# Performance work log

Hardware: AMD Instinct MI355X
Metric: run time of the kernel (lower is better)

The kernel has to match this reference:

```python
import jax, jax.numpy as jnp
import numpy as np

MARGIN = 0.2
LAMBDA_LSE = 6.0
LAMBDA_SOFTMAX = 9.0
EPS = 1e-8


def setup_inputs() -> dict:
    key = jax.random.key(0)
    k1, k2, k3 = jax.random.split(key, 3)
    I, R, W, D = 128, 36, 24, 512
    images = jax.random.normal(k1, (I, R, D), dtype=jnp.float32)
    captions = jax.random.normal(k2, (I, W, D), dtype=jnp.float32)
    # ragged caption lengths in [4, 24]
    cap_lens = 4 + jax.random.randint(k3, (I,), 0, W - 3, dtype=jnp.int32)
    return {"images": images, "captions": captions, "cap_lens": cap_lens}


def _scan_t2i_loss(images, captions, cap_lens):
    # images: [I, R, D]; captions: [C, W, D]; cap_lens: [C]
    C, W, D = captions.shape
    wmask = jnp.arange(W)[None, :] < cap_lens[:, None]          # [C, W] valid-word mask

    # raw attention: bmm(context=images, query^T=caption) -> [C, I, R, W]
    attn = jnp.einsum('ird,cwd->cirw', images, captions)
    # clipped_l2norm: LeakyReLU(0.1) then l2-normalize over word axis;
    # zero padded words so norms match the per-caption sliced computation
    a = jnp.where(attn > 0, attn, 0.1 * attn) * wmask[:, None, None, :]
    a = a / (jnp.sqrt(jnp.sum(a * a, axis=3, keepdims=True)) + EPS)
    # softmax over regions (sourceL) with temperature lambda_softmax
    s = jax.nn.softmax(a * LAMBDA_SOFTMAX, axis=2)              # [C, I, R, W]
    # weighted context per word: [C, I, W, D]
    wei = jnp.einsum('cirw,ird->ciwd', s, images)

    cap = captions[:, None, :, :]                               # [C, 1, W, D]
    num = jnp.sum(cap * wei, axis=-1)                           # [C, I, W]
    den = jnp.clip(jnp.linalg.norm(cap, axis=-1) * jnp.linalg.norm(wei, axis=-1), EPS)
    cos = num / den                                             # [C, I, W]

    # LogSumExp aggregation over valid words
    neg = jnp.finfo(cos.dtype).min
    logits = jnp.where(wmask[:, None, :], cos * LAMBDA_LSE, neg)
    row_sim = jax.nn.logsumexp(logits, axis=-1) / LAMBDA_LSE    # [C, I]
    scores = row_sim.T                                          # [I, C] (image x caption)

    diag = jnp.diag(scores)[:, None]                            # [I, 1]
    cost_s = jnp.clip(MARGIN + scores - diag, 0.0)
    cost_im = jnp.clip(MARGIN + scores - diag.T, 0.0)
    eye = jnp.eye(scores.shape[0], dtype=bool)
    cost_s = jnp.where(eye, 0.0, cost_s)
    cost_im = jnp.where(eye, 0.0, cost_im)
    # max_violation=True: hardest negatives
    cost_s = jnp.max(cost_s, axis=1)
    cost_im = jnp.max(cost_im, axis=0)
    return jnp.sum(cost_s) + jnp.sum(cost_im)


def reference(images, captions, cap_lens):
    return _scan_t2i_loss(images, captions, cap_lens)
```

## Files before the change

### kernel.cpp

```cpp
#include <hip/hip_runtime.h>
#include <math.h>

#define I_N 128
#define C_N 128
#define R_N 36
#define W_N 24
#define D_N 512
#define M_N (I_N * R_N)
#define N_N (C_N * W_N)

typedef __attribute__((ext_vector_type(8))) short bf16x8;
typedef __attribute__((ext_vector_type(4))) float f32x4;
typedef __attribute__((ext_vector_type(8))) unsigned short u16x8;
typedef _Float16 f16x2 __attribute__((ext_vector_type(2)));
typedef __fp16 h16x2 __attribute__((ext_vector_type(2)));

__device__ inline float bf2f(unsigned short u) {
    return __uint_as_float(((unsigned int)u) << 16);
}
__device__ inline unsigned short f2bf(float f) {
    unsigned int u = __float_as_uint(f);
    u = (u + 0x7FFFu + ((u >> 16) & 1u)) >> 16;
    return (unsigned short)u;
}
__device__ inline void gload_lds16(const void* g, void* l) {
    __builtin_amdgcn_global_load_lds(
        (const __attribute__((address_space(1))) void*)g,
        (__attribute__((address_space(3))) void*)l, 16, 0, 0);
}

#if __has_builtin(__builtin_amdgcn_fdot2)
__device__ inline float fdot2f(f16x2 a, f16x2 b, float c) {
    return __builtin_amdgcn_fdot2(__builtin_bit_cast(h16x2, a),
                                  __builtin_bit_cast(h16x2, b), c, false);
}
#else
__device__ inline float fdot2f(f16x2 a, f16x2 b, float c) {
    return c + (float)a[0] * (float)b[0] + (float)a[1] * (float)b[1];
}
#endif

#if __has_builtin(__builtin_amdgcn_cvt_pkrtz)
__device__ inline f16x2 pkf16(float a, float b) {
    return __builtin_bit_cast(f16x2, __builtin_amdgcn_cvt_pkrtz(a, b));
}
#else
__device__ inline f16x2 pkf16(float a, float b) {
    f16x2 v; v[0] = (_Float16)a; v[1] = (_Float16)b; return v;
}
#endif

__global__ __launch_bounds__(256) void convert_kernel(const float* __restrict__ images,
                                                      const float* __restrict__ captions,
                                                      unsigned short* __restrict__ imgbf,
                                                      unsigned short* __restrict__ capbf,
                                                      float* __restrict__ capn) {
    const int bid = blockIdx.x;
    if (bid < 1152) {
        int idx = bid * 256 + threadIdx.x;
        float4 v0 = *(const float4*)(images + (size_t)idx * 8);
        float4 v1 = *(const float4*)(images + (size_t)idx * 8 + 4);
        u16x8 o;
        o[0] = f2bf(v0.x); o[1] = f2bf(v0.y); o[2] = f2bf(v0.z); o[3] = f2bf(v0.w);
        o[4] = f2bf(v1.x); o[5] = f2bf(v1.y); o[6] = f2bf(v1.z); o[7] = f2bf(v1.w);
        *(u16x8*)(imgbf + (size_t)idx * 8) = o;
    } else {
        const int crow = (bid - 1152) * 4 + (threadIdx.x >> 6);
        const int lane = threadIdx.x & 63;
        const float* p = captions + (size_t)crow * D_N + lane * 8;
        float4 v0 = *(const float4*)p;
        float4 v1 = *(const float4*)(p + 4);
        u16x8 o;
        o[0] = f2bf(v0.x); o[1] = f2bf(v0.y); o[2] = f2bf(v0.z); o[3] = f2bf(v0.w);
        o[4] = f2bf(v1.x); o[5] = f2bf(v1.y); o[6] = f2bf(v1.z); o[7] = f2bf(v1.w);
        *(u16x8*)(capbf + (size_t)crow * D_N + lane * 8) = o;
        float s = v0.x*v0.x + v0.y*v0.y + v0.z*v0.z + v0.w*v0.w
                + v1.x*v1.x + v1.y*v1.y + v1.z*v1.z + v1.w*v1.w;
        #pragma unroll
        for (int off = 32; off > 0; off >>= 1) s += __shfl_down(s, off);
        if (lane == 0) capn[crow] = sqrtf(s);
    }
}

__global__ __launch_bounds__(256) void gram_kernel(const float* __restrict__ images,
                                                   unsigned int* __restrict__ G2) {
    __shared__ float tile[R_N][68];
    __shared__ float gshf[R_N][R_N];
    const int i = blockIdx.x;
    const float* img = images + (size_t)i * R_N * D_N;
    const int tid = threadIdx.x;
    const int t1 = (tid / 12) * 3;
    const int t2 = (tid % 12) * 3;
    const bool active = tid < 144;
    float acc[3][3] = {{0.f,0.f,0.f},{0.f,0.f,0.f},{0.f,0.f,0.f}};
    for (int k0 = 0; k0 < D_N; k0 += 64) {
        for (int idx = tid; idx < R_N * 16; idx += 256) {
            int r = idx / 16, k4 = idx % 16;
            float4 v = *(const float4*)(img + (size_t)r * D_N + k0 + k4 * 4);
            *(float4*)&tile[r][k4 * 4] = v;
        }
        __syncthreads();
        if (active) {
            #pragma unroll
            for (int k = 0; k < 64; k += 4) {
                float4 a0 = *(const float4*)&tile[t1 + 0][k];
                float4 a1 = *(const float4*)&tile[t1 + 1][k];
                float4 a2 = *(const float4*)&tile[t1 + 2][k];
                float4 b0 = *(const float4*)&tile[t2 + 0][k];
                float4 b1 = *(const float4*)&tile[t2 + 1][k];
                float4 b2 = *(const float4*)&tile[t2 + 2][k];
                acc[0][0] += a0.x*b0.x + a0.y*b0.y + a0.z*b0.z + a0.w*b0.w;
                acc[0][1] += a0.x*b1.x + a0.y*b1.y + a0.z*b1.z + a0.w*b1.w;
                acc[0][2] += a0.x*b2.x + a0.y*b2.y + a0.z*b2.z + a0.w*b2.w;
                acc[1][0] += a1.x*b0.x + a1.y*b0.y + a1.z*b0.z + a1.w*b0.w;
                acc[1][1] += a1.x*b1.x + a1.y*b1.y + a1.z*b1.z + a1.w*b1.w;
                acc[1][2] += a1.x*b2.x + a1.y*b2.y + a1.z*b2.z + a1.w*b2.w;
                acc[2][0] += a2.x*b0.x + a2.y*b0.y + a2.z*b0.z + a2.w*b0.w;
                acc[2][1] += a2.x*b1.x + a2.y*b1.y + a2.z*b1.z + a2.w*b1.w;
                acc[2][2] += a2.x*b2.x + a2.y*b2.y + a2.z*b2.z + a2.w*b2.w;
            }
        }
        __syncthreads();
    }
    if (active) {
        #pragma unroll
        for (int a = 0; a < 3; ++a)
            #pragma unroll
            for (int b = 0; b < 3; ++b)
                gshf[t1 + a][t2 + b] = acc[a][b];
    }
    __syncthreads();
    unsigned int* gp = G2 + (size_t)i * (R_N * 18);
    for (int idx = tid; idx < R_N * 18; idx += 256) {
        int r = idx / 18, p = idx % 18;
        gp[idx] = __builtin_bit_cast(unsigned int, pkf16(gshf[r][2 * p], gshf[r][2 * p + 1]));
    }
}

#define BM 128
#define BN 128
#define BK 32
#define KT (D_N / BK)
#define GX (M_N / BM)
#define GY (N_N / BN)

__global__ __launch_bounds__(256, 4) void attn_gemm_kernel(const unsigned short* __restrict__ A,
                                                           const unsigned short* __restrict__ B,
                                                           unsigned short* __restrict__ attn) {
    __shared__ unsigned short AsBuf[2][BM * BK];
    __shared__ unsigned short BsBuf[2][BN * BK];
    const int flat = blockIdx.x;
    const int nf = (flat & 7) * (GX * GY / 8) + (flat >> 3);
    const int m0 = (nf / GY) * BM;
    const int n0 = (nf % GY) * BN;
    const int tid = threadIdx.x;
    const int lane = tid & 63;
    const int wid = tid >> 6;
    const int wr = wid >> 1, wc = wid & 1;
    const int fr = lane & 15;
    const int fk = lane >> 4;

    const int srow = tid >> 2;
    const int sslot = (tid & 3) ^ (srow & 3);
    const unsigned short* srcA = A + (size_t)(m0 + srow) * D_N + sslot * 8;
    const unsigned short* srcB = B + (size_t)(n0 + srow) * D_N + sslot * 8;
    const int ldst = tid * 16;

    f32x4 acc[4][4];
    #pragma unroll
    for (int m = 0; m < 4; ++m)
        #pragma unroll
        for (int n = 0; n < 4; ++n) acc[m][n] = (f32x4){0.f, 0.f, 0.f, 0.f};

    #define STAGE(t, buf)                                                              \
        {                                                                              \
            const unsigned short* _a = srcA + (t) * BK;                                \
            const unsigned short* _b = srcB + (t) * BK;                                \
            gload_lds16(_a, (char*)AsBuf[buf] + ldst);                                 \
            gload_lds16(_a + (size_t)64 * D_N, (char*)AsBuf[buf] + 4096 + ldst);       \
            gload_lds16(_b, (char*)BsBuf[buf] + ldst);                                 \
            gload_lds16(_b + (size_t)64 * D_N, (char*)BsBuf[buf] + 4096 + ldst);       \
        }

    STAGE(0, 0)
    STAGE(1, 1)
    asm volatile("s_waitcnt vmcnt(4)" ::: "memory");
    __builtin_amdgcn_sched_barrier(0);
    __builtin_amdgcn_s_barrier();
    __builtin_amdgcn_sched_barrier(0);

    #pragma unroll
    for (int t = 0; t < KT; ++t) {
        const int cur = t & 1;
        const unsigned short* As = AsBuf[cur];
        const unsigned short* Bs = BsBuf[cur];
        bf16x8 af[4], bfr[4];
        #pragma unroll
        for (int m = 0; m < 4; ++m) {
            int rl = wr * 64 + m * 16 + fr;
            int byt = rl * 64 + ((fk ^ (fr & 3)) << 4);
            af[m] = *(const bf16x8*)((const char*)As + byt);
        }
        #pragma unroll
        for (int n = 0; n < 4; ++n) {
            int rl = wc * 64 + n * 16 + fr;
            int byt = rl * 64 + ((fk ^ (fr & 3)) << 4);
            bfr[n] = *(const bf16x8*)((const char*)Bs + byt);
        }
        #pragma unroll
        for (int m = 0; m < 4; ++m)
            #pragma unroll
            for (int n = 0; n < 4; ++n)
                acc[m][n] = __builtin_amdgcn_mfma_f32_16x16x32_bf16(af[m], bfr[n], acc[m][n], 0, 0, 0);
        __builtin_amdgcn_sched_barrier(0);
        __builtin_amdgcn_s_barrier();
        __builtin_amdgcn_sched_barrier(0);
        if (t + 2 < KT) STAGE(t + 2, cur)
        if (t + 1 < KT) {
            if (t + 2 < KT) {
                asm volatile("s_waitcnt vmcnt(4)" ::: "memory");
            } else {
                asm volatile("s_waitcnt vmcnt(0)" ::: "memory");
            }
            __builtin_amdgcn_sched_barrier(0);
            __builtin_amdgcn_s_barrier();
            __builtin_amdgcn_sched_barrier(0);
        }
    }
    #undef STAGE

    #pragma unroll
    for (int m = 0; m < 4; ++m) {
        #pragma unroll
        for (int n = 0; n < 4; ++n) {
            #pragma unroll
            for (int j = 0; j < 4; ++j) {
                int row = m0 + wr * 64 + m * 16 + fk * 4 + j;
                int col = n0 + wc * 64 + n * 16 + fr;
                int i = row / R_N, r = row - i * R_N;
                int c = col / W_N, w = col - c * W_N;
                attn[(((size_t)i * C_N + c) * R_N + r) * W_N + w] = f2bf(acc[m][n][j]);
            }
        }
    }
}

#define CG 8
#define SCL9 12.98425537f

__global__ __launch_bounds__(192) void score_kernel(const unsigned short* __restrict__ attn,
                                                    const unsigned int* __restrict__ G2,
                                                    const float* __restrict__ capn,
                                                    const int* __restrict__ cap_lens,
                                                    float* __restrict__ scores) {
    __shared__ unsigned short stage[CG * R_N * W_N];
    __shared__ unsigned int gsh2[R_N * 18];
    __shared__ float scl_sh[CG * R_N];
    __shared__ float red[CG][W_N];
    __shared__ int len_sh[CG];
    const int i = blockIdx.x;
    const int c0 = blockIdx.y * CG;
    const int tid = threadIdx.x;

    if (tid < CG) len_sh[tid] = cap_lens[c0 + tid];
    const unsigned short* at = attn + ((size_t)i * C_N + c0) * R_N * W_N;
    for (int ch = tid; ch < CG * R_N * W_N / 8; ch += 192)
        *(u16x8*)&stage[ch * 8] = *(const u16x8*)(at + ch * 8);
    const unsigned int* gp = G2 + (size_t)i * (R_N * 18);
    for (int idx = tid; idx < R_N * 18 / 2; idx += 192)
        *(uint2*)&gsh2[idx * 2] = *(const uint2*)(gp + idx * 2);
    __syncthreads();

    for (int row = tid; row < CG * R_N; row += 192) {
        int cl = row / R_N;
        int len = len_sh[cl];
        const unsigned short* rp = &stage[row * W_N];
        u16x8 p0 = *(const u16x8*)&rp[0];
        u16x8 p1 = *(const u16x8*)&rp[8];
        u16x8 p2 = *(const u16x8*)&rp[16];
        float ss = 0.f;
        #pragma unroll
        for (int q = 0; q < 8; ++q) {
            float x0 = bf2f(p0[q]); x0 = x0 > 0.f ? x0 : 0.1f * x0; x0 = (q      < len) ? x0 : 0.f;
            float x1 = bf2f(p1[q]); x1 = x1 > 0.f ? x1 : 0.1f * x1; x1 = (q + 8  < len) ? x1 : 0.f;
            float x2 = bf2f(p2[q]); x2 = x2 > 0.f ? x2 : 0.1f * x2; x2 = (q + 16 < len) ? x2 : 0.f;
            ss += x0 * x0 + x1 * x1 + x2 * x2;
        }
        scl_sh[row] = SCL9 / (sqrtf(ss) + 1e-8f);
    }
    __syncthreads();

    {
        const int cl = tid / W_N, w = tid - cl * W_N;
        const int len = len_sh[cl];
        const bool valid = w < len;
        const unsigned short* sb = &stage[cl * R_N * W_N];
        const float* sclp = &scl_sh[cl * R_N];
        f16x2 ep[18];
        float Z = 0.f, nu = 0.f;
        float e_prev = 0.f;
        #pragma unroll
        for (int r = 0; r < R_N; ++r) {
            float raw = bf2f(sb[r * W_N + w]);
            float x = raw > 0.f ? raw : 0.1f * raw;
            float l = valid ? x * sclp[r] : 0.f;
            float e = exp2f(l);
            Z += e;
            nu += e * raw;
            if (r & 1) ep[r >> 1] = pkf16(e_prev, e);
            else e_prev = e;
        }
        float wn = 0.f;
        #pragma unroll
        for (int r2 = 0; r2 < R_N; ++r2) {
            const unsigned int* grow = &gsh2[r2 * 18];
            float t0 = 0.f, t1 = 0.f;
            #pragma unroll
            for (int p = 0; p < 18; ++p) {
                f16x2 g = __builtin_bit_cast(f16x2, grow[p]);
                if (p & 1) t1 = fdot2f(g, ep[p], t1);
                else       t0 = fdot2f(g, ep[p], t0);
            }
            wn += (t0 + t1) * (float)ep[r2 >> 1][r2 & 1];
        }
        float iZ = 1.f / Z;
        float cn = capn[(c0 + cl) * W_N + w];
        float den = fmaxf(cn * sqrtf(fmaxf(wn, 0.f)) * iZ, 1e-8f);
        red[cl][w] = valid ? (nu * iZ) / den * 6.0f : -3.4e38f;
    }
    __syncthreads();
    if (tid < CG) {
        float se = 0.f;
        #pragma unroll
        for (int w = 0; w < W_N; ++w) se += __expf(red[tid][w] - 6.0f);
        scores[(size_t)(c0 + tid) * I_N + i] = (__logf(se) + 6.0f) / 6.0f;
    }
}

__global__ __launch_bounds__(128) void final_kernel(const float* __restrict__ scores,
                                                    float* __restrict__ out) {
    __shared__ float diag[C_N];
    __shared__ float red[C_N];
    const int t = threadIdx.x;
    diag[t] = scores[t * C_N + t];
    __syncthreads();
    const float di = diag[t];
    float cs = 0.f, cim = 0.f;
    for (int k = 0; k < C_N; ++k) {
        if (k == t) continue;
        float vs = 0.2f + scores[k * C_N + t] - di;
        float vi = 0.2f + scores[t * C_N + k] - di;
        cs = fmaxf(cs, vs);
        cim = fmaxf(cim, vi);
    }
    red[t] = cs + cim;
    __syncthreads();
    #pragma unroll
    for (int off = 64; off > 0; off >>= 1) {
        if (t < off) red[t] += red[t + off];
        __syncthreads();
    }
    if (t == 0) out[0] = red[0];
}

extern "C" void kernel_launch(void* const* d_in, const int* in_sizes, int n_in,
                              void* d_out, int out_size, void* d_ws, size_t ws_size,
                              hipStream_t stream) {
    (void)in_sizes; (void)n_in; (void)out_size; (void)ws_size;
    const float* images = (const float*)d_in[0];
    const float* captions = (const float*)d_in[1];
    const int* cap_lens = (const int*)d_in[2];
    float* out = (float*)d_out;

    char* wsb = (char*)d_ws;
    size_t off = 0;
    auto alloc = [&](size_t bytes) -> char* {
        char* p = wsb + off;
        off += (bytes + 255) & ~(size_t)255;
        return p;
    };
    unsigned short* imgbf = (unsigned short*)alloc((size_t)M_N * D_N * 2);
    unsigned short* capbf = (unsigned short*)alloc((size_t)N_N * D_N * 2);
    unsigned int* G2 = (unsigned int*)alloc((size_t)I_N * R_N * 18 * 4);
    float* capn = (float*)alloc((size_t)C_N * W_N * 4);
    float* scores = (float*)alloc((size_t)C_N * I_N * 4);
    unsigned short* attn = (unsigned short*)alloc((size_t)I_N * C_N * R_N * W_N * 2);

    convert_kernel<<<1920, 256, 0, stream>>>(images, captions, imgbf, capbf, capn);
    gram_kernel<<<I_N, 256, 0, stream>>>(images, G2);
    attn_gemm_kernel<<<GX * GY, 256, 0, stream>>>(imgbf, capbf, attn);
    score_kernel<<<dim3(I_N, C_N / CG), 192, 0, stream>>>(attn, G2, capn, cap_lens, scores);
    final_kernel<<<1, 128, 0, stream>>>(scores, out);
}
```

Measured before the change: 118.1 us.

## Fuse attention GEMM with score computation, keeping attention tile in shared memory

Merges the attention GEMM and score kernels into one kernel. Each block computes a 144x192 tile covering 4 images by 8 captions, writes the bf16 result to LDS, and then runs normalization, softmax, the weighted-norm and the LSE reduction in place, so the large attention tensor is never written to or read back from global memory. The Gram rows are padded to 20 words so they can be read with vector loads. The tradeoff is a larger LDS footprint (about 79 KB) and higher register pressure from 27 accumulators and three words per thread, which drops occupancy to 2 blocks. The per-wave vmcnt waits are also made uneven to match the extra A loads issued by wave 0.

After: 350.2 us. +196.4%, slower.

```diff
diff --git a/kernel.cpp b/kernel.cpp
--- a/kernel.cpp
+++ b/kernel.cpp
@@ -130,61 +130,94 @@
                 gshf[t1 + a][t2 + b] = acc[a][b];
     }
     __syncthreads();
-    unsigned int* gp = G2 + (size_t)i * (R_N * 18);
-    for (int idx = tid; idx < R_N * 18; idx += 256) {
-        int r = idx / 18, p = idx % 18;
-        gp[idx] = __builtin_bit_cast(unsigned int, pkf16(gshf[r][2 * p], gshf[r][2 * p + 1]));
-    }
-}
-
-#define BM 128
-#define BN 128
+    unsigned int* gp = G2 + (size_t)i * (R_N * 20);
+    for (int idx = tid; idx < R_N * 20; idx += 256) {
+        int r = idx / 20, p = idx % 20;
+        f16x2 v;
+        if (p < 18) v = pkf16(gshf[r][2 * p], gshf[r][2 * p + 1]);
+        else { v[0] = (_Float16)0.f; v[1] = (_Float16)0.f; }
+        gp[idx] = __builtin_bit_cast(unsigned int, v);
+    }
+}
+
 #define BK 32
 #define KT (D_N / BK)
-#define GX (M_N / BM)
-#define GY (N_N / BN)
-
-__global__ __launch_bounds__(256, 4) void attn_gemm_kernel(const unsigned short* __restrict__ A,
-                                                           const unsigned short* __restrict__ B,
-                                                           unsigned short* __restrict__ attn) {
-    __shared__ unsigned short AsBuf[2][BM * BK];
-    __shared__ unsigned short BsBuf[2][BN * BK];
+#define OUT_OFF 0
+#define GSH_OFF 59904
+#define SCL_OFF 71424
+#define RED_OFF 76032
+#define LEN_OFF 79104
+#define SMEM_SZ 79168
+#define SCL9 12.98425537f
+
+__global__ __launch_bounds__(256, 2) void attn_score_kernel(const unsigned short* __restrict__ A,
+                                                            const unsigned short* __restrict__ B,
+                                                            const unsigned int* __restrict__ G2,
+                                                            const float* __restrict__ capn,
+                                                            const int* __restrict__ cap_lens,
+                                                            float* __restrict__ scores) {
+    __shared__ char smem[SMEM_SZ];
     const int flat = blockIdx.x;
-    const int nf = (flat & 7) * (GX * GY / 8) + (flat >> 3);
-    const int m0 = (nf / GY) * BM;
-    const int n0 = (nf % GY) * BN;
+    const int nf = (flat & 7) * 64 + (flat >> 3);
+    const int IG = nf >> 4;
+    const int CGp = nf & 15;
+    const int i0 = IG * 4;
+    const int cap0 = CGp * 8;
     const int tid = threadIdx.x;
     const int lane = tid & 63;
     const int wid = tid >> 6;
-    const int wr = wid >> 1, wc = wid & 1;
     const int fr = lane & 15;
     const int fk = lane >> 4;
 
-    const int srow = tid >> 2;
-    const int sslot = (tid & 3) ^ (srow & 3);
-    const unsigned short* srcA = A + (size_t)(m0 + srow) * D_N + sslot * 8;
-    const unsigned short* srcB = B + (size_t)(n0 + srow) * D_N + sslot * 8;
-    const int ldst = tid * 16;
-
-    f32x4 acc[4][4];
+    const unsigned short* Abase = A + (size_t)(IG * 144) * D_N;
+    const unsigned short* Bbase = B + (size_t)(CGp * 192) * D_N;
+
+    {
+        const unsigned int* gsrc = G2 + (size_t)i0 * (R_N * 20);
+        unsigned int* gdst = (unsigned int*)(smem + GSH_OFF);
+        #pragma unroll
+        for (int k = 0; k < 12; ++k) {
+            int idx = tid + k * 256;
+            if (idx < 2880) gdst[idx] = gsrc[idx];
+        }
+        if (tid < 8) ((int*)(smem + LEN_OFF))[tid] = cap_lens[cap0 + tid];
+    }
+    asm volatile("s_waitcnt vmcnt(0)" ::: "memory");
+    __builtin_amdgcn_sched_barrier(0);
+
+    f32x4 acc[9][3];
     #pragma unroll
-    for (int m = 0; m < 4; ++m)
-        #pragma unroll
-        for (int n = 0; n < 4; ++n) acc[m][n] = (f32x4){0.f, 0.f, 0.f, 0.f};
-
-    #define STAGE(t, buf)                                                              \
-        {                                                                              \
-            const unsigned short* _a = srcA + (t) * BK;                                \
-            const unsigned short* _b = srcB + (t) * BK;                                \
-            gload_lds16(_a, (char*)AsBuf[buf] + ldst);                                 \
-            gload_lds16(_a + (size_t)64 * D_N, (char*)AsBuf[buf] + 4096 + ldst);       \
-            gload_lds16(_b, (char*)BsBuf[buf] + ldst);                                 \
-            gload_lds16(_b + (size_t)64 * D_N, (char*)BsBuf[buf] + 4096 + ldst);       \
-        }
+    for (int m = 0; m < 9; ++m)
+        #pragma unroll
+        for (int n = 0; n < 3; ++n) acc[m][n] = (f32x4){0.f, 0.f, 0.f, 0.f};
+
+    #define STAGE(t, buf)                                                         \
+        {                                                                         \
+            const int kk = (t) * BK;                                              \
+            _Pragma("unroll")                                                     \
+            for (int k = 0; k < 3; ++k) {                                         \
+                int ch = tid + k * 256;                                           \
+                if (ch < 576) {                                                   \
+                    int row = ch >> 2, swz = (ch & 3) ^ (row & 3);                \
+                    gload_lds16(Abase + (size_t)row * D_N + kk + swz * 8,         \
+                                smem + (buf) * 9216 + ch * 16);                   \
+                }                                                                 \
+            }                                                                     \
+            _Pragma("unroll")                                                     \
+            for (int k = 0; k < 3; ++k) {                                         \
+                int ch = tid + k * 256;                                           \
+                int row = ch >> 2, swz = (ch & 3) ^ (row & 3);                    \
+                gload_lds16(Bbase + (size_t)row * D_N + kk + swz * 8,             \
+                            smem + 18432 + (buf) * 12288 + ch * 16);              \
+            }                                                                     \
+        }
+    #define WAIT_TILE                                                             \
+        if (wid == 0) { asm volatile("s_waitcnt vmcnt(6)" ::: "memory"); }        \
+        else          { asm volatile("s_waitcnt vmcnt(5)" ::: "memory"); }
 
     STAGE(0, 0)
     STAGE(1, 1)
-    asm volatile("s_waitcnt vmcnt(4)" ::: "memory");
+    WAIT_TILE
     __builtin_amdgcn_sched_barrier(0);
     __builtin_amdgcn_s_barrier();
     __builtin_amdgcn_sched_barrier(0);
@@ -192,25 +225,23 @@
     #pragma unroll
     for (int t = 0; t < KT; ++t) {
         const int cur = t & 1;
-        const unsigned short* As = AsBuf[cur];
-        const unsigned short* Bs = BsBuf[cur];
-        bf16x8 af[4], bfr[4];
-        #pragma unroll
-        for (int m = 0; m < 4; ++m) {
-            int rl = wr * 64 + m * 16 + fr;
-            int byt = rl * 64 + ((fk ^ (fr & 3)) << 4);
-            af[m] = *(const bf16x8*)((const char*)As + byt);
-        }
-        #pragma unroll
-        for (int n = 0; n < 4; ++n) {
-            int rl = wc * 64 + n * 16 + fr;
-            int byt = rl * 64 + ((fk ^ (fr & 3)) << 4);
-            bfr[n] = *(const bf16x8*)((const char*)Bs + byt);
-        }
-        #pragma unroll
-        for (int m = 0; m < 4; ++m)
+        const char* As = smem + cur * 9216;
+        const char* Bs = smem + 18432 + cur * 12288;
+        bf16x8 af[9], bfr[3];
+        #pragma unroll
+        for (int m = 0; m < 9; ++m) {
+            int rl = m * 16 + fr;
+            af[m] = *(const bf16x8*)(As + rl * 64 + ((fk ^ (fr & 3)) << 4));
+        }
+        #pragma unroll
+        for (int n = 0; n < 3; ++n) {
+            int rl = (wid * 3 + n) * 16 + fr;
+            bfr[n] = *(const bf16x8*)(Bs + rl * 64 + ((fk ^ (fr & 3)) << 4));
+        }
+        #pragma unroll
+        for (int m = 0; m < 9; ++m)
             #pragma unroll
-            for (int n = 0; n < 4; ++n)
+            for (int n = 0; n < 3; ++n)
                 acc[m][n] = __builtin_amdgcn_mfma_f32_16x16x32_bf16(af[m], bfr[n], acc[m][n], 0, 0, 0);
         __builtin_amdgcn_sched_barrier(0);
         __builtin_amdgcn_s_barrier();
@@ -218,7 +249,7 @@
         if (t + 2 < KT) STAGE(t + 2, cur)
         if (t + 1 < KT) {
             if (t + 2 < KT) {
-                asm volatile("s_waitcnt vmcnt(4)" ::: "memory");
+                WAIT_TILE
             } else {
                 asm volatile("s_waitcnt vmcnt(0)" ::: "memory");
             }
@@ -228,53 +259,28 @@
         }
     }
     #undef STAGE
-
+    #undef WAIT_TILE
+
+    unsigned short* outT = (unsigned short*)(smem + OUT_OFF);
     #pragma unroll
-    for (int m = 0; m < 4; ++m) {
-        #pragma unroll
-        for (int n = 0; n < 4; ++n) {
+    for (int m = 0; m < 9; ++m)
+        #pragma unroll
+        for (int n = 0; n < 3; ++n)
             #pragma unroll
             for (int j = 0; j < 4; ++j) {
-                int row = m0 + wr * 64 + m * 16 + fk * 4 + j;
-                int col = n0 + wc * 64 + n * 16 + fr;
-                int i = row / R_N, r = row - i * R_N;
-                int c = col / W_N, w = col - c * W_N;
-                attn[(((size_t)i * C_N + c) * R_N + r) * W_N + w] = f2bf(acc[m][n][j]);
+                int row = m * 16 + fk * 4 + j;
+                int col = (wid * 3 + n) * 16 + fr;
+                outT[row * 208 + col] = f2bf(acc[m][n][j]);
             }
-        }
-    }
-}
-
-#define CG 8
-#define SCL9 12.98425537f
-
-__global__ __launch_bounds__(192) void score_kernel(const unsigned short* __restrict__ attn,
-                                                    const unsigned int* __restrict__ G2,
-                                                    const float* __restrict__ capn,
-                                                    const int* __restrict__ cap_lens,
-                                                    float* __restrict__ scores) {
-    __shared__ unsigned short stage[CG * R_N * W_N];
-    __shared__ unsigned int gsh2[R_N * 18];
-    __shared__ float scl_sh[CG * R_N];
-    __shared__ float red[CG][W_N];
-    __shared__ int len_sh[CG];
-    const int i = blockIdx.x;
-    const int c0 = blockIdx.y * CG;
-    const int tid = threadIdx.x;
-
-    if (tid < CG) len_sh[tid] = cap_lens[c0 + tid];
-    const unsigned short* at = attn + ((size_t)i * C_N + c0) * R_N * W_N;
-    for (int ch = tid; ch < CG * R_N * W_N / 8; ch += 192)
-        *(u16x8*)&stage[ch * 8] = *(const u16x8*)(at + ch * 8);
-    const unsigned int* gp = G2 + (size_t)i * (R_N * 18);
-    for (int idx = tid; idx < R_N * 18 / 2; idx += 192)
-        *(uint2*)&gsh2[idx * 2] = *(const uint2*)(gp + idx * 2);
-    __syncthreads();
-
-    for (int row = tid; row < CG * R_N; row += 192) {
-        int cl = row / R_N;
-        int len = len_sh[cl];
-        const unsigned short* rp = &stage[row * W_N];
+    __syncthreads();
+
+    const int* lenp = (const int*)(smem + LEN_OFF);
+    float* scl = (float*)(smem + SCL_OFF);
+    for (int fl = tid; fl < 1152; fl += 256) {
+        int i = fl / 288, rem = fl - i * 288;
+        int c = rem / 36, r = rem - c * 36;
+        int len = lenp[c];
+        const unsigned short* rp = outT + (i * 36 + r) * 208 + c * 24;
         u16x8 p0 = *(const u16x8*)&rp[0];
         u16x8 p1 = *(const u16x8*)&rp[8];
         u16x8 p2 = *(const u16x8*)&rp[16];
@@ -286,54 +292,83 @@
             float x2 = bf2f(p2[q]); x2 = x2 > 0.f ? x2 : 0.1f * x2; x2 = (q + 16 < len) ? x2 : 0.f;
             ss += x0 * x0 + x1 * x1 + x2 * x2;
         }
-        scl_sh[row] = SCL9 / (sqrtf(ss) + 1e-8f);
+        scl[fl] = SCL9 / (sqrtf(ss) + 1e-8f);
     }
     __syncthreads();
 
     {
-        const int cl = tid / W_N, w = tid - cl * W_N;
-        const int len = len_sh[cl];
-        const bool valid = w < len;
-        const unsigned short* sb = &stage[cl * R_N * W_N];
-        const float* sclp = &scl_sh[cl * R_N];
-        f16x2 ep[18];
-        float Z = 0.f, nu = 0.f;
-        float e_prev = 0.f;
+        const int i_loc = wid;
+        const unsigned int* gbase = (const unsigned int*)(smem + GSH_OFF) + i_loc * (R_N * 20);
+        const float* sclb = scl + i_loc * 288;
+        float* redb = (float*)(smem + RED_OFF);
+        const int cA = lane / 24,          wA = lane - cA * 24;
+        const int cB = (lane + 64) / 24,   wB = (lane + 64) - cB * 24;
+        const int cC = (lane + 128) / 24,  wC = (lane + 128) - cC * 24;
+        const bool vA = wA < lenp[cA], vB = wB < lenp[cB], vC = wC < lenp[cC];
+        const unsigned short* tb = outT + i_loc * 36 * 208;
+
+        f16x2 epA[18], epB[18], epC[18];
+        float ZA = 0.f, ZB = 0.f, ZC = 0.f, nuA = 0.f, nuB = 0.f, nuC = 0.f;
+        float eA_p = 0.f, eB_p = 0.f, eC_p = 0.f;
         #pragma unroll
         for (int r = 0; r < R_N; ++r) {
-            float raw = bf2f(sb[r * W_N + w]);
-            float x = raw > 0.f ? raw : 0.1f * raw;
-            float l = valid ? x * sclp[r] : 0.f;
-            float e = exp2f(l);
-            Z += e;
-            nu += e * raw;
-            if (r & 1) ep[r >> 1] = pkf16(e_prev, e);
-            else e_prev = e;
-        }
-        float wn = 0.f;
+            float rawA = bf2f(tb[r * 208 + lane]);
+            float rawB = bf2f(tb[r * 208 + lane + 64]);
+            float rawC = bf2f(tb[r * 208 + lane + 128]);
+            float xA = rawA > 0.f ? rawA : 0.1f * rawA;
+            float xB = rawB > 0.f ? rawB : 0.1f * rawB;
+            float xC = rawC > 0.f ? rawC : 0.1f * rawC;
+            float lA = vA ? xA * sclb[cA * 36 + r] : 0.f;
+            float lB = vB ? xB * sclb[cB * 36 + r] : 0.f;
+            float lC = vC ? xC * sclb[cC * 36 + r] : 0.f;
+            float eA = exp2f(lA), eB = exp2f(lB), eC = exp2f(lC);
+            ZA += eA; ZB += eB; ZC += eC;
+            nuA += eA * rawA; nuB += eB * rawB; nuC += eC * rawC;
+            if (r & 1) {
+                epA[r >> 1] = pkf16(eA_p, eA);
+                epB[r >> 1] = pkf16(eB_p, eB);
+                epC[r >> 1] = pkf16(eC_p, eC);
+            } else { eA_p = eA; eB_p = eB; eC_p = eC; }
+        }
+        float wnA = 0.f, wnB = 0.f, wnC = 0.f;
         #pragma unroll
         for (int r2 = 0; r2 < R_N; ++r2) {
-            const unsigned int* grow = &gsh2[r2 * 18];
-            float t0 = 0.f, t1 = 0.f;
+            const unsigned int* grow = gbase + r2 * 20;
+            uint4 q0 = *(const uint4*)(grow + 0);
+            uint4 q1 = *(const uint4*)(grow + 4);
+            uint4 q2 = *(const uint4*)(grow + 8);
+            uint4 q3 = *(const uint4*)(grow + 12);
+            uint2 q4 = *(const uint2*)(grow + 16);
+            unsigned int gq[18] = {q0.x, q0.y, q0.z, q0.w, q1.x, q1.y, q1.z, q1.w,
+                                   q2.x, q2.y, q2.z, q2.w, q3.x, q3.y, q3.z, q3.w,
+                                   q4.x, q4.y};
+            float tA0 = 0.f, tA1 = 0.f, tB0 = 0.f, tB1 = 0.f, tC0 = 0.f, tC1 = 0.f;
             #pragma unroll
             for (int p = 0; p < 18; ++p) {
-                f16x2 g = __builtin_bit_cast(f16x2, grow[p]);
-                if (p & 1) t1 = fdot2f(g, ep[p], t1);
-                else       t0 = fdot2f(g, ep[p], t0);
+                f16x2 g = __builtin_bit_cast(f16x2, gq[p]);
+                if (p & 1) { tA1 = fdot2f(g, epA[p], tA1); tB1 = fdot2f(g, epB[p], tB1); tC1 = fdot2f(g, epC[p], tC1); }
+                else       { tA0 = fdot2f(g, epA[p], tA0); tB0 = fdot2f(g, epB[p], tB0); tC0 = fdot2f(g, epC[p], tC0); }
             }
-            wn += (t0 + t1) * (float)ep[r2 >> 1][r2 & 1];
-        }
-        float iZ = 1.f / Z;
-        float cn = capn[(c0 + cl) * W_N + w];
-        float den = fmaxf(cn * sqrtf(fmaxf(wn, 0.f)) * iZ, 1e-8f);
-        red[cl][w] = valid ? (nu * iZ) / den * 6.0f : -3.4e38f;
-    }
-    __syncthreads();
-    if (tid < CG) {
+            wnA += (tA0 + tA1) * (float)epA[r2 >> 1][r2 & 1];
+            wnB += (tB0 + tB1) * (float)epB[r2 >> 1][r2 & 1];
+            wnC += (tC0 + tC1) * (float)epC[r2 >> 1][r2 & 1];
+        }
+        float iZA = 1.f / ZA, iZB = 1.f / ZB, iZC = 1.f / ZC;
+        float dnA = fmaxf(capn[(cap0 + cA) * W_N + wA] * sqrtf(fmaxf(wnA, 0.f)) * iZA, 1e-8f);
+        float dnB = fmaxf(capn[(cap0 + cB) * W_N + wB] * sqrtf(fmaxf(wnB, 0.f)) * iZB, 1e-8f);
+        float dnC = fmaxf(capn[(cap0 + cC) * W_N + wC] * sqrtf(fmaxf(wnC, 0.f)) * iZC, 1e-8f);
+        redb[(i_loc * 8 + cA) * W_N + wA] = vA ? (nuA * iZA) / dnA * 6.0f : -3.4e38f;
+        redb[(i_loc * 8 + cB) * W_N + wB] = vB ? (nuB * iZB) / dnB * 6.0f : -3.4e38f;
+        redb[(i_loc * 8 + cC) * W_N + wC] = vC ? (nuC * iZC) / dnC * 6.0f : -3.4e38f;
+    }
+    __syncthreads();
+    if (tid < 32) {
+        const float* redb = (const float*)(smem + RED_OFF);
+        int i = tid >> 3, c = tid & 7;
         float se = 0.f;
         #pragma unroll
-        for (int w = 0; w < W_N; ++w) se += __expf(red[tid][w] - 6.0f);
-        scores[(size_t)(c0 + tid) * I_N + i] = (__logf(se) + 6.0f) / 6.0f;
+        for (int w = 0; w < W_N; ++w) se += __expf(redb[tid * W_N + w] - 6.0f);
+        scores[(size_t)(cap0 + c) * I_N + (i0 + i)] = (__logf(se) + 6.0f) / 6.0f;
     }
 }
 
@@ -381,14 +416,12 @@
     };
     unsigned short* imgbf = (unsigned short*)alloc((size_t)M_N * D_N * 2);
     unsigned short* capbf = (unsigned short*)alloc((size_t)N_N * D_N * 2);
-    unsigned int* G2 = (unsigned int*)alloc((size_t)I_N * R_N * 18 * 4);
+    unsigned int* G2 = (unsigned int*)alloc((size_t)I_N * R_N * 20 * 4);
     float* capn = (float*)alloc((size_t)C_N * W_N * 4);
     float* scores = (float*)alloc((size_t)C_N * I_N * 4);
-    unsigned short* attn = (unsigned short*)alloc((size_t)I_N * C_N * R_N * W_N * 2);
 
     convert_kernel<<<1920, 256, 0, stream>>>(images, captions, imgbf, capbf, capn);
     gram_kernel<<<I_N, 256, 0, stream>>>(images, G2);
-    attn_gemm_kernel<<<GX * GY, 256, 0, stream>>>(imgbf, capbf, attn);
-    score_kernel<<<dim3(I_N, C_N / CG), 192, 0, stream>>>(attn, G2, capn, cap_lens, scores);
+    attn_score_kernel<<<512, 256, 0, stream>>>(imgbf, capbf, G2, capn, cap_lens, scores);
     final_kernel<<<1, 128, 0, stream>>>(scores, out);
 }
```
